# Kernel optimization log

Measured on AMD Instinct MI355X. Metric: run time of the kernel, lower is better.

Reference implementation:

```python
import jax, jax.numpy as jnp
import numpy as np
import math


def setup_inputs() -> dict:
    key = jax.random.key(0)
    k_x, k_q, k_k, k_v, k_o = jax.random.split(key, 5)
    B, S, D_IN, H, D_K, D_V, D_OUT = 1, 4096, 512, 8, 64, 64, 512
    # torch.rand -> uniform[0,1); scaled by 0.02 to keep softmax unsaturated
    scale = 0.02
    return {
        "x": jax.random.normal(k_x, (B, S, D_IN), dtype=jnp.float32),
        "W_q": jax.random.uniform(k_q, (H, D_IN, D_K), dtype=jnp.float32) * scale,
        "W_k": jax.random.uniform(k_k, (H, D_IN, D_K), dtype=jnp.float32) * scale,
        "W_v": jax.random.uniform(k_v, (H, D_IN, D_V), dtype=jnp.float32) * scale,
        "W_o": jax.random.uniform(k_o, (H, D_V, D_OUT), dtype=jnp.float32) * scale,
    }


def reference(x, W_q, W_k, W_v, W_o):
    # x: [B,S,d_in]; W_q/W_k: [H,d_in,d_k]; W_v: [H,d_in,d_v]; W_o: [H,d_v,d_out]
    S = x.shape[-2]
    d_key = W_k.shape[-1]
    Q = jnp.einsum('hjk,blj->bhlk', W_q, x)   # [B,H,S,d_k]
    K = jnp.einsum('hjk,blj->bhlk', W_k, x)   # [B,H,S,d_k]
    V = jnp.einsum('hjk,blj->bhlk', W_v, x)   # [B,H,S,d_v]
    # causal mask: True where masked (strict upper triangle)
    mask = jnp.triu(jnp.ones((S, S), dtype=bool), k=1)  # [S,S]
    scores = jnp.einsum('bhik,bhjk->bhij', Q, K)        # [B,H,S,S]
    scores = jnp.where(mask, -jnp.inf, scores)
    # is_scaled=True: divide by sqrt(d_key) before softmax
    weights = jax.nn.softmax(scores / math.sqrt(d_key), axis=-1)
    weights = jnp.where(mask, 0.0, weights)
    values = jnp.einsum('bhij,bhjv->bhiv', weights, V)  # [B,H,S,d_v]
    return jnp.einsum('hvk,bhlv->blk', W_o, values)     # [B,S,d_out]
```

## Files before the change

### kernel.cpp

```cpp
#include <hip/hip_runtime.h>
#include <hip/hip_bf16.h>
#include <math.h>

#define S_LEN 4096
#define NH    8

typedef __attribute__((ext_vector_type(8))) short bf16x8;
typedef __attribute__((ext_vector_type(4))) short bf16x4;
typedef __attribute__((ext_vector_type(4))) float f32x4;
typedef __attribute__((ext_vector_type(16))) float f32x16;
typedef __attribute__((ext_vector_type(2)))  int   int32x2;
typedef __attribute__((ext_vector_type(4)))  unsigned short u16x4;

#define QSCALE 0.18033688011112042f

#define WAIT_VM6 0x0F76
#define WAIT_VM4 0x0F74
#define WAIT_VM0 0x0F70

__device__ __forceinline__ short f2bf(float f) {
    union { float f; unsigned u; } v; v.f = f;
    unsigned r = v.u + 0x7fffu + ((v.u >> 16) & 1u);
    return (short)(r >> 16);
}

__device__ __forceinline__ float bf2f(unsigned short s) {
    union { unsigned u; float f; } v; v.u = ((unsigned)s) << 16; return v.f;
}

__device__ __forceinline__ int pk2(float a, float b) {
    __hip_bfloat162 t = __float22bfloat162_rn(make_float2(a, b));
    union { __hip_bfloat162 h; int i; } u; u.h = t;
    return u.i;
}

__device__ __forceinline__ void gload16(const void* g, void* l) {
    __builtin_amdgcn_global_load_lds(
        (const __attribute__((address_space(1))) unsigned*)g,
        (__attribute__((address_space(3))) unsigned*)l, 16, 0, 0);
}

__device__ __forceinline__ void stage_tile(const short* gsrc, size_t gstride,
                                           short* tile, int t)
{
    const int wave = t >> 6, lane = t & 63;
    const int sub = lane >> 3;
    const int cg  = (lane & 7) ^ sub;
#pragma unroll
    for (int j = 0; j < 2; ++j) {
        const int chunk = wave * 2 + j;
        const int row = chunk * 8 + sub;
        gload16(gsrc + (size_t)row * gstride + cg * 8, tile + chunk * 512);
    }
}

__device__ __forceinline__ bf16x8 frag(const short* tile, int row, int cg) {
    return *(const bf16x8*)&tile[row * 64 + ((cg ^ (row & 7)) << 3)];
}

__device__ __forceinline__ bf16x8 mk_bp(const f32x16& sc, const int p, float& lsum)
{
    const float e0 = __builtin_amdgcn_exp2f(sc[8 * p + 0]);
    const float e1 = __builtin_amdgcn_exp2f(sc[8 * p + 1]);
    const float e2 = __builtin_amdgcn_exp2f(sc[8 * p + 2]);
    const float e3 = __builtin_amdgcn_exp2f(sc[8 * p + 3]);
    const float e4 = __builtin_amdgcn_exp2f(sc[8 * p + 4]);
    const float e5 = __builtin_amdgcn_exp2f(sc[8 * p + 5]);
    const float e6 = __builtin_amdgcn_exp2f(sc[8 * p + 6]);
    const float e7 = __builtin_amdgcn_exp2f(sc[8 * p + 7]);
    lsum += ((e0 + e1) + (e2 + e3)) + ((e4 + e5) + (e6 + e7));
    int we0 = pk2(e0, e1), we1 = pk2(e2, e3);
    int wo0 = pk2(e4, e5), wo1 = pk2(e6, e7);
    const int32x2 r0 = __builtin_amdgcn_permlane32_swap(we0, wo0, false, false);
    const int32x2 r1 = __builtin_amdgcn_permlane32_swap(we1, wo1, false, false);
    union { int i[4]; bf16x8 v; } u;
    u.i[0] = r0[0]; u.i[1] = r1[0]; u.i[2] = r0[1]; u.i[3] = r1[1];
    return u.v;
}

__device__ __forceinline__ void gemm_mainloop_512(
    const short* __restrict__ Arow, const short* __restrict__ Brow,
    short* As, short* Bs, f32x4 acc[4], int t)
{
    const int wave = t >> 6, lane = t & 63, n16 = lane & 15, quad = lane >> 4;
    stage_tile(Arow, 512, As, t);
    stage_tile(Brow, 512, Bs, t);
    for (int c = 0; c < 8; ++c) {
        const int cur = c & 1;
        __builtin_amdgcn_s_barrier();
        if (c < 7) {
            stage_tile(Arow + (c + 1) * 64, 512, As + (1 - cur) * 4096, t);
            stage_tile(Brow + (c + 1) * 64, 512, Bs + (1 - cur) * 4096, t);
            __builtin_amdgcn_s_waitcnt(WAIT_VM4);
        } else {
            __builtin_amdgcn_s_waitcnt(WAIT_VM0);
        }
        __builtin_amdgcn_s_barrier();
        const short* as = As + cur * 4096;
        const short* bs = Bs + cur * 4096;
#pragma unroll
        for (int kh = 0; kh < 2; ++kh) {
            const bf16x8 a = frag(as, wave * 16 + n16, kh * 4 + quad);
#pragma unroll
            for (int nt = 0; nt < 4; ++nt) {
                const bf16x8 b = frag(bs, nt * 16 + n16, kh * 4 + quad);
                acc[nt] = __builtin_amdgcn_mfma_f32_16x16x32_bf16(a, b, acc[nt], 0, 0, 0);
            }
        }
    }
}

__global__ __launch_bounds__(256) void prep_kernel(
    const float* __restrict__ x,
    const float* __restrict__ Wq, const float* __restrict__ Wk,
    const float* __restrict__ Wv, const float* __restrict__ Wo,
    short* __restrict__ xb, short* __restrict__ Wqkvt, short* __restrict__ Wot)
{
    __shared__ short T[64 * 66];
    const int b = blockIdx.x, t = threadIdx.x;
    if (b < 1024) {
        const size_t idx = (size_t)b * 2048 + t * 8;
        const float4 a = *(const float4*)&x[idx];
        const float4 c = *(const float4*)&x[idx + 4];
        bf16x8 o;
        o[0] = f2bf(a.x); o[1] = f2bf(a.y); o[2] = f2bf(a.z); o[3] = f2bf(a.w);
        o[4] = f2bf(c.x); o[5] = f2bf(c.y); o[6] = f2bf(c.z); o[7] = f2bf(c.w);
        *(bf16x8*)&xb[idx] = o;
        return;
    }
    const int c4 = (t & 15) * 4, rsub = t >> 4;
    const int orow = t >> 2, oc16 = (t & 3) * 16;
    if (b < 1216) {
        const int jj = b - 1024, g = jj >> 3, kb = jj & 7;
        const int which = g >> 3, h = g & 7;
        const float* W = ((which == 0) ? Wq : (which == 1) ? Wk : Wv) + (size_t)h * 512 * 64;
#pragma unroll
        for (int p = 0; p < 4; ++p) {
            const int row = p * 16 + rsub;
            const float4 v = *(const float4*)&W[(size_t)(kb * 64 + row) * 64 + c4];
            T[(c4 + 0) * 66 + row] = f2bf(v.x);
            T[(c4 + 1) * 66 + row] = f2bf(v.y);
            T[(c4 + 2) * 66 + row] = f2bf(v.z);
            T[(c4 + 3) * 66 + row] = f2bf(v.w);
        }
        __syncthreads();
        short* O = &Wqkvt[((size_t)g * 64 + orow) * 512 + kb * 64];
        *(bf16x8*)&O[oc16]     = *(const bf16x8*)&T[orow * 66 + oc16];
        *(bf16x8*)&O[oc16 + 8] = *(const bf16x8*)&T[orow * 66 + oc16 + 8];
    } else {
        const int jj = b - 1216, h = jj >> 3, nb = jj & 7;
        const float* W = Wo + (size_t)h * 64 * 512;
#pragma unroll
        for (int p = 0; p < 4; ++p) {
            const int row = p * 16 + rsub;
            const float4 v = *(const float4*)&W[(size_t)row * 512 + nb * 64 + c4];
            T[(c4 + 0) * 66 + row] = f2bf(v.x);
            T[(c4 + 1) * 66 + row] = f2bf(v.y);
            T[(c4 + 2) * 66 + row] = f2bf(v.z);
            T[(c4 + 3) * 66 + row] = f2bf(v.w);
        }
        __syncthreads();
        short* O = &Wot[((size_t)nb * 64 + orow) * 512 + h * 64];
        *(bf16x8*)&O[oc16]     = *(const bf16x8*)&T[orow * 66 + oc16];
        *(bf16x8*)&O[oc16 + 8] = *(const bf16x8*)&T[orow * 66 + oc16 + 8];
    }
}

__global__ __launch_bounds__(256) void qkv_gemm_kernel(
    const short* __restrict__ xb, const short* __restrict__ Wqkvt,
    short* __restrict__ Qg, short* __restrict__ Kg, short* __restrict__ Vtg)
{
    __shared__ short smem[24576];
    short* As = smem;
    short* Bs = smem + 16384;
    const int sblk = blockIdx.x, g = blockIdx.y;
    const int which = g >> 3, h = g & 7;
    const int t = threadIdx.x;
    const int wave = t >> 6, lane = t & 63, n16 = lane & 15, quad = lane >> 4;

    const short* Arow = xb + (size_t)sblk * 128 * 512;
    const short* Brow = Wqkvt + (size_t)g * 64 * 512;

    f32x4 acc[2][4] = {{{0,0,0,0},{0,0,0,0},{0,0,0,0},{0,0,0,0}},
                       {{0,0,0,0},{0,0,0,0},{0,0,0,0},{0,0,0,0}}};

    stage_tile(Arow,            512, As,        t);
    stage_tile(Arow + 64 * 512, 512, As + 4096, t);
    stage_tile(Brow,            512, Bs,        t);
    for (int c = 0; c < 8; ++c) {
        const int cur = c & 1;
        __builtin_amdgcn_s_barrier();
        if (c < 7) {
            stage_tile(Arow + (c + 1) * 64,            512, As + (1 - cur) * 8192,        t);
            stage_tile(Arow + 64 * 512 + (c + 1) * 64, 512, As + (1 - cur) * 8192 + 4096, t);
            stage_tile(Brow + (c + 1) * 64,            512, Bs + (1 - cur) * 4096,        t);
            __builtin_amdgcn_s_waitcnt(WAIT_VM6);
        } else {
            __builtin_amdgcn_s_waitcnt(WAIT_VM0);
        }
        __builtin_amdgcn_s_barrier();
        const short* as = As + cur * 8192;
        const short* bs = Bs + cur * 4096;
        const int r0 = wave * 32 + n16;
        const short* a_sub = as + (r0 >> 6) * 4096;
#pragma unroll
        for (int kh = 0; kh < 2; ++kh) {
            const bf16x8 a0 = frag(a_sub, r0 & 63,        kh * 4 + quad);
            const bf16x8 a1 = frag(a_sub, (r0 & 63) + 16, kh * 4 + quad);
#pragma unroll
            for (int nt = 0; nt < 4; ++nt) {
                const bf16x8 b = frag(bs, nt * 16 + n16, kh * 4 + quad);
                acc[0][nt] = __builtin_amdgcn_mfma_f32_16x16x32_bf16(a0, b, acc[0][nt], 0, 0, 0);
                acc[1][nt] = __builtin_amdgcn_mfma_f32_16x16x32_bf16(a1, b, acc[1][nt], 0, 0, 0);
            }
        }
    }

    if (which < 2) {
        const float scale = (which == 0) ? QSCALE : 1.0f;
        short* O = ((which == 0) ? Qg : Kg) + (size_t)h * S_LEN * 64;
#pragma unroll
        for (int m = 0; m < 2; ++m)
#pragma unroll
            for (int nt = 0; nt < 4; ++nt)
#pragma unroll
                for (int r = 0; r < 4; ++r) {
                    const int s = sblk * 128 + wave * 32 + m * 16 + quad * 4 + r;
                    O[(size_t)s * 64 + nt * 16 + n16] = f2bf(acc[m][nt][r] * scale);
                }
    } else {
        __syncthreads();
        short* Tr = smem;
#pragma unroll
        for (int m = 0; m < 2; ++m)
#pragma unroll
            for (int nt = 0; nt < 4; ++nt)
#pragma unroll
                for (int r = 0; r < 4; ++r)
                    Tr[(nt * 16 + n16) * 130 + wave * 32 + m * 16 + quad * 4 + r] =
                        f2bf(acc[m][nt][r]);
        __syncthreads();
        short* O = Vtg + (size_t)h * 64 * S_LEN + sblk * 128;
        const int vr = t >> 2, c32 = (t & 3) * 32;
#pragma unroll
        for (int u = 0; u < 4; ++u)
            *(bf16x8*)&O[(size_t)vr * S_LEN + c32 + u * 8] =
                *(const bf16x8*)&Tr[vr * 130 + c32 + u * 8];
    }
}

__global__ __launch_bounds__(256) void out_gemm_kernel(
    const short* __restrict__ vals, const short* __restrict__ Wot, float* __restrict__ out)
{
    __shared__ short smem[16384];
    short* As = smem;
    short* Bs = smem + 8192;
    const int sblk = blockIdx.x, g = blockIdx.y;
    const int t = threadIdx.x;
    const int wave = t >> 6, lane = t & 63, n16 = lane & 15, quad = lane >> 4;

    f32x4 acc[4] = {{0,0,0,0},{0,0,0,0},{0,0,0,0},{0,0,0,0}};
    gemm_mainloop_512(vals + (size_t)sblk * 64 * 512, Wot + (size_t)g * 64 * 512,
                      As, Bs, acc, t);

#pragma unroll
    for (int nt = 0; nt < 4; ++nt)
#pragma unroll
        for (int r = 0; r < 4; ++r) {
            const int s = sblk * 64 + wave * 16 + quad * 4 + r;
            out[(size_t)s * 512 + g * 64 + nt * 16 + n16] = acc[nt][r];
        }
}

__global__ __launch_bounds__(256, 3) void attn_kernel(
    const short* __restrict__ Qg, const short* __restrict__ Kg,
    const short* __restrict__ Vtg, short* __restrict__ Opart, float* __restrict__ Lpart)
{
    __shared__ short Ks[2][4096];
    __shared__ short Vs[2][4096];

    const int id = blockIdx.x;
    const int h  = id & 7;
    const int cc = 95 - (id >> 3);
    int qs, j;
    if (cc < 6)       { qs = cc;                    j = 0; }
    else if (cc < 20) { qs = 6  + ((cc - 6) >> 1);  j = (cc - 6) & 1; }
    else if (cc < 38) { qs = 13 + (cc - 20) / 3;    j = (cc - 20) % 3; }
    else if (cc < 66) { qs = 19 + ((cc - 38) >> 2); j = (cc - 38) & 3; }
    else              { qs = 26 + (cc - 66) / 5;    j = (cc - 66) % 5; }
    const int k0   = j * 13;
    const int kend = min(k0 + 13, 2 * qs + 2);

    const short* Kh  = Kg  + (size_t)h * S_LEN * 64;
    const short* Vth = Vtg + (size_t)h * 64 * S_LEN;

    const int t = threadIdx.x;
    const int wave = t >> 6, lane = t & 63, l31 = lane & 31, half = lane >> 5;
    const int qg = qs * 128 + wave * 32 + l31;

    const short* Qr = Qg + (size_t)h * S_LEN * 64 + (size_t)qg * 64;
    bf16x8 bq[4];
#pragma unroll
    for (int kc = 0; kc < 4; ++kc)
        bq[kc] = *(const bf16x8*)&Qr[kc * 16 + half * 8];

    f32x16 z16;
#pragma unroll
    for (int r = 0; r < 16; ++r) z16[r] = 0.f;

    f32x16 oacc[2];
#pragma unroll
    for (int r = 0; r < 16; ++r) { oacc[0][r] = 0.f; oacc[1][r] = 0.f; }
    float llane = 0.f;

    stage_tile(Kh + (size_t)k0 * 64 * 64, 64, Ks[0], t);
    stage_tile(Vth + k0 * 64, S_LEN, Vs[0], t);

    for (int kb = k0; kb < kend; ++kb) {
        const int cur = (kb - k0) & 1;
        __builtin_amdgcn_s_barrier();
        if (kb + 1 < kend) {
            stage_tile(Kh + (size_t)(kb + 1) * 64 * 64, 64, Ks[1 - cur], t);
            stage_tile(Vth + (kb + 1) * 64, S_LEN, Vs[1 - cur], t);
            __builtin_amdgcn_s_waitcnt(WAIT_VM4);
        } else {
            __builtin_amdgcn_s_waitcnt(WAIT_VM0);
        }
        __builtin_amdgcn_s_barrier();

        __builtin_amdgcn_s_setprio(1);
        f32x16 sc0, sc1;
        {
            const bf16x8 a0 = frag(Ks[cur], l31,      half);
            const bf16x8 a1 = frag(Ks[cur], 32 + l31, half);
            sc0 = __builtin_amdgcn_mfma_f32_32x32x16_bf16(a0, bq[0], z16, 0, 0, 0);
            sc1 = __builtin_amdgcn_mfma_f32_32x32x16_bf16(a1, bq[0], z16, 0, 0, 0);
        }
#pragma unroll
        for (int kc = 1; kc < 4; ++kc) {
            const bf16x8 a0 = frag(Ks[cur], l31,      kc * 2 + half);
            const bf16x8 a1 = frag(Ks[cur], 32 + l31, kc * 2 + half);
            sc0 = __builtin_amdgcn_mfma_f32_32x32x16_bf16(a0, bq[kc], sc0, 0, 0, 0);
            sc1 = __builtin_amdgcn_mfma_f32_32x32x16_bf16(a1, bq[kc], sc1, 0, 0, 0);
        }
        __builtin_amdgcn_s_setprio(0);

        if (kb * 64 + 63 > qg) {
#pragma unroll
            for (int r = 0; r < 16; ++r) {
                const int keyb = kb * 64 + (r & 3) + 8 * (r >> 2) + 4 * half;
                if (keyb > qg)      sc0[r] = -1e30f;
                if (keyb + 32 > qg) sc1[r] = -1e30f;
            }
        }

        bf16x8 bp[4];
        bp[0] = mk_bp(sc0, 0, llane);
        bp[1] = mk_bp(sc0, 1, llane);
        bp[2] = mk_bp(sc1, 0, llane);
        bp[3] = mk_bp(sc1, 1, llane);

        __builtin_amdgcn_s_setprio(1);
#pragma unroll
        for (int kc = 0; kc < 4; ++kc) {
            const bf16x8 a0 = frag(Vs[cur], l31,      kc * 2 + half);
            const bf16x8 a1 = frag(Vs[cur], 32 + l31, kc * 2 + half);
            oacc[0] = __builtin_amdgcn_mfma_f32_32x32x16_bf16(a0, bp[kc], oacc[0], 0, 0, 0);
            oacc[1] = __builtin_amdgcn_mfma_f32_32x32x16_bf16(a1, bp[kc], oacc[1], 0, 0, 0);
        }
        __builtin_amdgcn_s_setprio(0);
    }

    short* tileO = Opart + (size_t)(h * 96 + cc) * (64 * 128);
    float* tileL = Lpart + (h * 96 + cc) * 128;
    const float lq = llane + __shfl_xor(llane, 32, 64);
    if (half == 0) tileL[wave * 32 + l31] = lq;
#pragma unroll
    for (int mt = 0; mt < 2; ++mt)
#pragma unroll
        for (int r = 0; r < 16; ++r) {
            const int v = mt * 32 + (r & 3) + 8 * (r >> 2) + 4 * half;
            tileO[(v << 7) + wave * 32 + l31] = f2bf(mt ? oacc[1][r] : oacc[0][r]);
        }
}

__global__ __launch_bounds__(256) void combine_norm_kernel(
    const short* __restrict__ Opart, const float* __restrict__ Lpart,
    short* __restrict__ vals)
{
    __shared__ short T[128 * 66];
    const int id = blockIdx.x;
    const int h = id & 7, qs = id >> 3;
    int c0, nj;
    if (qs < 6)       { c0 = qs;                 nj = 1; }
    else if (qs < 13) { c0 = 6  + 2 * (qs - 6);  nj = 2; }
    else if (qs < 19) { c0 = 20 + 3 * (qs - 13); nj = 3; }
    else if (qs < 26) { c0 = 38 + 4 * (qs - 19); nj = 4; }
    else              { c0 = 66 + 5 * (qs - 26); nj = 5; }
    const int base = h * 96 + c0;

    const int t = threadIdx.x;
    const int q0 = (t & 31) * 4;
    const int vr = t >> 5;

    f32x4 L = {0, 0, 0, 0};
    for (int j = 0; j < nj; ++j)
        L += *(const f32x4*)&Lpart[(base + j) * 128 + q0];
    const f32x4 inv = {1.f / L[0], 1.f / L[1], 1.f / L[2], 1.f / L[3]};

#pragma unroll
    for (int pass = 0; pass < 8; ++pass) {
        const int v = vr + pass * 8;
        f32x4 s = {0, 0, 0, 0};
        for (int j = 0; j < nj; ++j) {
            const u16x4 u = *(const u16x4*)&Opart[(size_t)(base + j) * 8192 + (v << 7) + q0];
            s[0] += bf2f(u[0]); s[1] += bf2f(u[1]);
            s[2] += bf2f(u[2]); s[3] += bf2f(u[3]);
        }
        T[(q0 + 0) * 66 + v] = f2bf(s[0] * inv[0]);
        T[(q0 + 1) * 66 + v] = f2bf(s[1] * inv[1]);
        T[(q0 + 2) * 66 + v] = f2bf(s[2] * inv[2]);
        T[(q0 + 3) * 66 + v] = f2bf(s[3] * inv[3]);
    }
    __syncthreads();
    const int q = t >> 1, vh = (t & 1) * 32;
    const size_t row = (size_t)(qs * 128 + q) * 512 + h * 64 + vh;
#pragma unroll
    for (int u = 0; u < 4; ++u)
        *(bf16x8*)&vals[row + u * 8] = *(const bf16x8*)&T[q * 66 + vh + u * 8];
}

extern "C" void kernel_launch(void* const* d_in, const int* in_sizes, int n_in,
                              void* d_out, int out_size, void* d_ws, size_t ws_size,
                              hipStream_t stream)
{
    const float* x  = (const float*)d_in[0];
    const float* Wq = (const float*)d_in[1];
    const float* Wk = (const float*)d_in[2];
    const float* Wv = (const float*)d_in[3];
    const float* Wo = (const float*)d_in[4];
    float* out = (float*)d_out;

    short* xb    = (short*)d_ws;
    short* Wqkvt = xb + 2097152;
    short* Wot   = Wqkvt + 786432;
    short* Qg    = Wot + 262144;
    short* Kg    = Qg + 2097152;
    short* Vtg   = Kg + 2097152;
    short* vals  = Vtg + 2097152;
    short* Opart = vals + 2097152;
    float* Lpart = (float*)(Opart + (size_t)768 * 8192);

    prep_kernel<<<1280, 256, 0, stream>>>(x, Wq, Wk, Wv, Wo, xb, Wqkvt, Wot);
    qkv_gemm_kernel<<<dim3(32, 24), 256, 0, stream>>>(xb, Wqkvt, Qg, Kg, Vtg);
    attn_kernel<<<768, 256, 0, stream>>>(Qg, Kg, Vtg, Opart, Lpart);
    combine_norm_kernel<<<256, 256, 0, stream>>>(Opart, Lpart, vals);
    out_gemm_kernel<<<dim3(64, 8), 256, 0, stream>>>(vals, Wot, out);
}
```

Measured before the change: 133.1 us.

## Fuse QKV+attention and combine+out-proj kernels using global atomic counters

```diff
diff --git a/kernel.cpp b/kernel.cpp
--- a/kernel.cpp
+++ b/kernel.cpp
@@ -110,14 +110,13 @@
     }
 }
 
-__global__ __launch_bounds__(256) void prep_kernel(
+__device__ __forceinline__ void prep_body(
+    int b, int t, short* T,
     const float* __restrict__ x,
     const float* __restrict__ Wq, const float* __restrict__ Wk,
     const float* __restrict__ Wv, const float* __restrict__ Wo,
     short* __restrict__ xb, short* __restrict__ Wqkvt, short* __restrict__ Wot)
 {
-    __shared__ short T[64 * 66];
-    const int b = blockIdx.x, t = threadIdx.x;
     if (b < 1024) {
         const size_t idx = (size_t)b * 2048 + t * 8;
         const float4 a = *(const float4*)&x[idx];
@@ -166,16 +165,14 @@
     }
 }
 
-__global__ __launch_bounds__(256) void qkv_gemm_kernel(
+__device__ __forceinline__ void qkv_body(
+    int sblk, int g, int t, short* smem,
     const short* __restrict__ xb, const short* __restrict__ Wqkvt,
     short* __restrict__ Qg, short* __restrict__ Kg, short* __restrict__ Vtg)
 {
-    __shared__ short smem[24576];
     short* As = smem;
     short* Bs = smem + 16384;
-    const int sblk = blockIdx.x, g = blockIdx.y;
     const int which = g >> 3, h = g & 7;
-    const int t = threadIdx.x;
     const int wave = t >> 6, lane = t & 63, n16 = lane & 15, quad = lane >> 4;
 
     const short* Arow = xb + (size_t)sblk * 128 * 512;
@@ -249,37 +246,12 @@
     }
 }
 
-__global__ __launch_bounds__(256) void out_gemm_kernel(
-    const short* __restrict__ vals, const short* __restrict__ Wot, float* __restrict__ out)
-{
-    __shared__ short smem[16384];
-    short* As = smem;
-    short* Bs = smem + 8192;
-    const int sblk = blockIdx.x, g = blockIdx.y;
-    const int t = threadIdx.x;
-    const int wave = t >> 6, lane = t & 63, n16 = lane & 15, quad = lane >> 4;
-
-    f32x4 acc[4] = {{0,0,0,0},{0,0,0,0},{0,0,0,0},{0,0,0,0}};
-    gemm_mainloop_512(vals + (size_t)sblk * 64 * 512, Wot + (size_t)g * 64 * 512,
-                      As, Bs, acc, t);
-
-#pragma unroll
-    for (int nt = 0; nt < 4; ++nt)
-#pragma unroll
-        for (int r = 0; r < 4; ++r) {
-            const int s = sblk * 64 + wave * 16 + quad * 4 + r;
-            out[(size_t)s * 512 + g * 64 + nt * 16 + n16] = acc[nt][r];
-        }
-}
-
-__global__ __launch_bounds__(256, 3) void attn_kernel(
+__device__ __forceinline__ void attn_body(
+    int id, int t, short* smem,
     const short* __restrict__ Qg, const short* __restrict__ Kg,
-    const short* __restrict__ Vtg, short* __restrict__ Opart, float* __restrict__ Lpart)
-{
-    __shared__ short Ks[2][4096];
-    __shared__ short Vs[2][4096];
-
-    const int id = blockIdx.x;
+    const short* __restrict__ Vtg, short* __restrict__ Opart,
+    float* __restrict__ Lpart)
+{
     const int h  = id & 7;
     const int cc = 95 - (id >> 3);
     int qs, j;
@@ -294,7 +266,6 @@
     const short* Kh  = Kg  + (size_t)h * S_LEN * 64;
     const short* Vth = Vtg + (size_t)h * 64 * S_LEN;
 
-    const int t = threadIdx.x;
     const int wave = t >> 6, lane = t & 63, l31 = lane & 31, half = lane >> 5;
     const int qg = qs * 128 + wave * 32 + l31;
 
@@ -313,15 +284,17 @@
     for (int r = 0; r < 16; ++r) { oacc[0][r] = 0.f; oacc[1][r] = 0.f; }
     float llane = 0.f;
 
-    stage_tile(Kh + (size_t)k0 * 64 * 64, 64, Ks[0], t);
-    stage_tile(Vth + k0 * 64, S_LEN, Vs[0], t);
+    stage_tile(Kh + (size_t)k0 * 64 * 64, 64, smem, t);
+    stage_tile(Vth + k0 * 64, S_LEN, smem + 8192, t);
 
     for (int kb = k0; kb < kend; ++kb) {
         const int cur = (kb - k0) & 1;
+        const short* Kc = smem + cur * 4096;
+        const short* Vc = smem + 8192 + cur * 4096;
         __builtin_amdgcn_s_barrier();
         if (kb + 1 < kend) {
-            stage_tile(Kh + (size_t)(kb + 1) * 64 * 64, 64, Ks[1 - cur], t);
-            stage_tile(Vth + (kb + 1) * 64, S_LEN, Vs[1 - cur], t);
+            stage_tile(Kh + (size_t)(kb + 1) * 64 * 64, 64, smem + (1 - cur) * 4096, t);
+            stage_tile(Vth + (kb + 1) * 64, S_LEN, smem + 8192 + (1 - cur) * 4096, t);
             __builtin_amdgcn_s_waitcnt(WAIT_VM4);
         } else {
             __builtin_amdgcn_s_waitcnt(WAIT_VM0);
@@ -331,15 +304,15 @@
         __builtin_amdgcn_s_setprio(1);
         f32x16 sc0, sc1;
         {
-            const bf16x8 a0 = frag(Ks[cur], l31,      half);
-            const bf16x8 a1 = frag(Ks[cur], 32 + l31, half);
+            const bf16x8 a0 = frag(Kc, l31,      half);
+            const bf16x8 a1 = frag(Kc, 32 + l31, half);
             sc0 = __builtin_amdgcn_mfma_f32_32x32x16_bf16(a0, bq[0], z16, 0, 0, 0);
             sc1 = __builtin_amdgcn_mfma_f32_32x32x16_bf16(a1, bq[0], z16, 0, 0, 0);
         }
 #pragma unroll
         for (int kc = 1; kc < 4; ++kc) {
-            const bf16x8 a0 = frag(Ks[cur], l31,      kc * 2 + half);
-            const bf16x8 a1 = frag(Ks[cur], 32 + l31, kc * 2 + half);
+            const bf16x8 a0 = frag(Kc, l31,      kc * 2 + half);
+            const bf16x8 a1 = frag(Kc, 32 + l31, kc * 2 + half);
             sc0 = __builtin_amdgcn_mfma_f32_32x32x16_bf16(a0, bq[kc], sc0, 0, 0, 0);
             sc1 = __builtin_amdgcn_mfma_f32_32x32x16_bf16(a1, bq[kc], sc1, 0, 0, 0);
         }
@@ -363,8 +336,8 @@
         __builtin_amdgcn_s_setprio(1);
 #pragma unroll
         for (int kc = 0; kc < 4; ++kc) {
-            const bf16x8 a0 = frag(Vs[cur], l31,      kc * 2 + half);
-            const bf16x8 a1 = frag(Vs[cur], 32 + l31, kc * 2 + half);
+            const bf16x8 a0 = frag(Vc, l31,      kc * 2 + half);
+            const bf16x8 a1 = frag(Vc, 32 + l31, kc * 2 + half);
             oacc[0] = __builtin_amdgcn_mfma_f32_32x32x16_bf16(a0, bp[kc], oacc[0], 0, 0, 0);
             oacc[1] = __builtin_amdgcn_mfma_f32_32x32x16_bf16(a1, bp[kc], oacc[1], 0, 0, 0);
         }
@@ -384,12 +357,11 @@
         }
 }
 
-__global__ __launch_bounds__(256) void combine_norm_kernel(
+__device__ __forceinline__ void combine_body(
+    int id, int t, short* T,
     const short* __restrict__ Opart, const float* __restrict__ Lpart,
     short* __restrict__ vals)
 {
-    __shared__ short T[128 * 66];
-    const int id = blockIdx.x;
     const int h = id & 7, qs = id >> 3;
     int c0, nj;
     if (qs < 6)       { c0 = qs;                 nj = 1; }
@@ -399,7 +371,6 @@
     else              { c0 = 66 + 5 * (qs - 26); nj = 5; }
     const int base = h * 96 + c0;
 
-    const int t = threadIdx.x;
     const int q0 = (t & 31) * 4;
     const int vr = t >> 5;
 
@@ -428,6 +399,90 @@
 #pragma unroll
     for (int u = 0; u < 4; ++u)
         *(bf16x8*)&vals[row + u * 8] = *(const bf16x8*)&T[q * 66 + vh + u * 8];
+}
+
+__device__ __forceinline__ void out_body(
+    int sblk, int g, int t, short* smem,
+    const short* __restrict__ vals, const short* __restrict__ Wot,
+    float* __restrict__ out)
+{
+    short* As = smem;
+    short* Bs = smem + 8192;
+    const int wave = t >> 6, lane = t & 63, n16 = lane & 15, quad = lane >> 4;
+
+    f32x4 acc[4] = {{0,0,0,0},{0,0,0,0},{0,0,0,0},{0,0,0,0}};
+    gemm_mainloop_512(vals + (size_t)sblk * 64 * 512, Wot + (size_t)g * 64 * 512,
+                      As, Bs, acc, t);
+
+#pragma unroll
+    for (int nt = 0; nt < 4; ++nt)
+#pragma unroll
+        for (int r = 0; r < 4; ++r) {
+            const int s = sblk * 64 + wave * 16 + quad * 4 + r;
+            out[(size_t)s * 512 + g * 64 + nt * 16 + n16] = acc[nt][r];
+        }
+}
+
+__global__ __launch_bounds__(256) void prep_kernel(
+    const float* __restrict__ x,
+    const float* __restrict__ Wq, const float* __restrict__ Wk,
+    const float* __restrict__ Wv, const float* __restrict__ Wo,
+    short* __restrict__ xb, short* __restrict__ Wqkvt, short* __restrict__ Wot,
+    int* __restrict__ counters)
+{
+    __shared__ short T[64 * 66];
+    if (blockIdx.x == 0 && threadIdx.x < 33) counters[threadIdx.x] = 0;
+    prep_body(blockIdx.x, threadIdx.x, T, x, Wq, Wk, Wv, Wo, xb, Wqkvt, Wot);
+}
+
+__global__ __launch_bounds__(256, 3) void qkv_attn_kernel(
+    const short* __restrict__ xb, const short* __restrict__ Wqkvt,
+    short* __restrict__ Qg, short* __restrict__ Kg, short* __restrict__ Vtg,
+    short* __restrict__ Opart, float* __restrict__ Lpart,
+    int* __restrict__ counters)
+{
+    __shared__ short smem[24576];
+    const int bid = blockIdx.x, t = threadIdx.x;
+
+    qkv_body(bid & 31, bid >> 5, t, smem, xb, Wqkvt, Qg, Kg, Vtg);
+
+    __threadfence();
+    __syncthreads();
+    if (t == 0) {
+        __hip_atomic_fetch_add(&counters[0], 1, __ATOMIC_RELEASE, __HIP_MEMORY_SCOPE_AGENT);
+        while (__hip_atomic_load(&counters[0], __ATOMIC_ACQUIRE, __HIP_MEMORY_SCOPE_AGENT) < 768)
+            __builtin_amdgcn_s_sleep(8);
+    }
+    __syncthreads();
+
+    attn_body(bid, t, smem, Qg, Kg, Vtg, Opart, Lpart);
+}
+
+__global__ __launch_bounds__(256, 2) void combine_out_kernel(
+    const short* __restrict__ Opart, const float* __restrict__ Lpart,
+    short* __restrict__ vals, const short* __restrict__ Wot,
+    float* __restrict__ out, int* __restrict__ counters)
+{
+    __shared__ short smem[16384];
+    const int bid = blockIdx.x, t = threadIdx.x;
+
+    if (bid < 256) {
+        combine_body(bid, t, smem, Opart, Lpart, vals);
+        __threadfence();
+        __syncthreads();
+        if (t == 0)
+            __hip_atomic_fetch_add(&counters[1 + (bid >> 3)], 1,
+                                   __ATOMIC_RELEASE, __HIP_MEMORY_SCOPE_AGENT);
+    }
+
+    const int sblk = bid & 63, g = bid >> 6;
+    if (t == 0)
+        while (__hip_atomic_load(&counters[1 + (sblk >> 1)],
+                                 __ATOMIC_ACQUIRE, __HIP_MEMORY_SCOPE_AGENT) < 8)
+            __builtin_amdgcn_s_sleep(8);
+    __syncthreads();
+
+    out_body(sblk, g, t, smem, vals, Wot, out);
 }
 
 extern "C" void kernel_launch(void* const* d_in, const int* in_sizes, int n_in,
@@ -450,10 +505,9 @@
     short* vals  = Vtg + 2097152;
     short* Opart = vals + 2097152;
     float* Lpart = (float*)(Opart + (size_t)768 * 8192);
-
-    prep_kernel<<<1280, 256, 0, stream>>>(x, Wq, Wk, Wv, Wo, xb, Wqkvt, Wot);
-    qkv_gemm_kernel<<<dim3(32, 24), 256, 0, stream>>>(xb, Wqkvt, Qg, Kg, Vtg);
-    attn_kernel<<<768, 256, 0, stream>>>(Qg, Kg, Vtg, Opart, Lpart);
-    combine_norm_kernel<<<256, 256, 0, stream>>>(Opart, Lpart, vals);
-    out_gemm_kernel<<<dim3(64, 8), 256, 0, stream>>>(vals, Wot, out);
-}
+    int* counters = (int*)(Lpart + 768 * 128);
+
+    prep_kernel<<<1280, 256, 0, stream>>>(x, Wq, Wk, Wv, Wo, xb, Wqkvt, Wot, counters);
+    qkv_attn_kernel<<<768, 256, 0, stream>>>(xb, Wqkvt, Qg, Kg, Vtg, Opart, Lpart, counters);
+    combine_out_kernel<<<512, 256, 0, stream>>>(Opart, Lpart, vals, Wot, out, counters);
+}
```

After: 415.3 us. 3.12x slower.
